# Performance work log

Measured on AMD Instinct MI355X. Metric: run time of the kernel, lower is better.

The kernel has to match this reference:

```python
import jax, jax.numpy as jnp
import numpy as np

B, H, W, C, E, TOP_K = 16, 64, 64, 384, 5, 2


def setup_inputs() -> dict:
    key = jax.random.key(0)
    k1, k2, k3 = jax.random.split(key, 3)
    x = jax.random.normal(k1, (B, H, W, C), dtype=jnp.float32)
    Wg = jax.random.normal(k2, (C, E), dtype=jnp.float32) * 0.02   # router
    We = jax.random.normal(k3, (E, C, C), dtype=jnp.float32) * 0.02  # expert weights
    be = jnp.zeros((E, C), dtype=jnp.float32)                       # expert biases
    return {"x": x, "Wg": Wg, "We": We, "be": be}


def reference(x, Wg, We, be):
    Bx, Hx, Wx, Cx = x.shape
    Ex = Wg.shape[1]
    t = x.reshape(-1, Cx)                      # [N, C] tokens
    N = t.shape[0]

    # --- top-k routing ---
    logits = t @ Wg                            # [N, E]
    top_vals, top_idx = jax.lax.top_k(logits, TOP_K)   # [N, 2]
    gates = jax.nn.softmax(top_vals, axis=-1)          # softmax over selected experts
    combine = jnp.zeros((N, Ex), dtype=t.dtype)
    combine = combine.at[jnp.arange(N)[:, None], top_idx].set(gates)  # [N, E] sparse combine weights

    # --- expert computation (dense over experts, combined with sparse gates) ---
    expert_out = jnp.einsum('nc,ecd->ned', t, We) + be[None]  # [N, E, C]
    y = jnp.einsum('ne,ned->nd', combine, expert_out)         # [N, C]

    # --- LeakyReLU (default slope 0.01); dropout is identity in eval mode ---
    y = jax.nn.leaky_relu(y, negative_slope=0.01)
    return y.reshape(Bx, Hx, Wx, Cx)
```

## Files before the change

kernel.cpp:

```cpp
#include <hip/hip_runtime.h>
#include <stdint.h>

#define TOKENS 65536
#define CDIM 384
#define NEXP 5
#define NPAIR 10
#define CAP 8192
#define NBLK 1024
#define WE_STRIDE (CDIM * CDIM)

typedef __attribute__((ext_vector_type(8))) short short8;
typedef __attribute__((ext_vector_type(4))) float floatx4;

__constant__ int PAIR_A[NPAIR] = {0, 0, 0, 0, 1, 1, 1, 2, 2, 3};
__constant__ int PAIR_B[NPAIR] = {1, 2, 3, 4, 2, 3, 4, 3, 4, 4};

__device__ inline unsigned short f2bf(float f) {
    union { float f; uint32_t u; } v; v.f = f;
    uint32_t r = v.u + 0x7fffu + ((v.u >> 16) & 1u);
    return (unsigned short)(r >> 16);
}

__device__ inline void load_lds16(const void* g, void* l) {
    __builtin_amdgcn_global_load_lds((const __attribute__((address_space(1))) void*)g,
                                     (__attribute__((address_space(3))) void*)l, 16, 0, 0);
}

__global__ __launch_bounds__(256) void router_kernel(const float* __restrict__ x,
                                                     const float* __restrict__ Wg,
                                                     int* __restrict__ blkcnt,
                                                     int* __restrict__ tmeta,
                                                     float2* __restrict__ tgate) {
    __shared__ __align__(16) float  wgs[CDIM * 8];
    __shared__ __align__(16) double part[4 * 64 * NEXP];
    __shared__ __align__(16) double lg[64 * NEXP];
    int t = threadIdx.x, lane = t & 63, w = t >> 6;
    int tok0 = blockIdx.x * 64;

    for (int i = t; i < CDIM * NEXP; i += 256) wgs[(i / NEXP) * 8 + (i % NEXP)] = Wg[i];
    __syncthreads();

    const float4* xb = (const float4*)(x + (size_t)(tok0 + lane) * CDIM + w * 96);
    double p0 = 0, p1 = 0, p2 = 0, p3 = 0, p4 = 0;
    #pragma unroll
    for (int i4 = 0; i4 < 24; ++i4) {
        float4 xv = xb[i4];
        #pragma unroll
        for (int u = 0; u < 4; ++u) {
            int c = w * 96 + i4 * 4 + u;
            float xe = (u == 0) ? xv.x : (u == 1) ? xv.y : (u == 2) ? xv.z : xv.w;
            float4 w03 = *(const float4*)&wgs[c * 8];
            float  w4  = wgs[c * 8 + 4];
            double xd = (double)xe;
            p0 += xd * w03.x; p1 += xd * w03.y; p2 += xd * w03.z;
            p3 += xd * w03.w; p4 += xd * w4;
        }
    }
    double* pr = &part[(w * 64 + lane) * NEXP];
    pr[0] = p0; pr[1] = p1; pr[2] = p2; pr[3] = p3; pr[4] = p4;
    __syncthreads();

    for (int item = t; item < 64 * NEXP; item += 256) {
        lg[item] = part[item] + part[320 + item] + part[640 + item] + part[960 + item];
    }
    __syncthreads();

    if (t < 64) {
        double pa[NEXP];
        #pragma unroll
        for (int e = 0; e < NEXP; ++e) pa[e] = lg[t * NEXP + e];
        int i0 = 0; double m0v = pa[0];
        #pragma unroll
        for (int e = 1; e < NEXP; ++e) if (pa[e] > m0v) { m0v = pa[e]; i0 = e; }
        int i1 = -1; double m1v = -1e300;
        #pragma unroll
        for (int e = 0; e < NEXP; ++e) if (e != i0 && pa[e] > m1v) { m1v = pa[e]; i1 = e; }
        float d  = (float)(m1v - m0v);
        float e1 = expf(d);
        float inv = 1.0f / (1.0f + e1);

        int a  = i0 < i1 ? i0 : i1;
        int b2 = i0 < i1 ? i1 : i0;
        int p  = a * 4 - ((a * (a - 1)) >> 1) + (b2 - a - 1);
        float ga = (a == i0) ? inv : e1 * inv;
        float gb = (a == i0) ? e1 * inv : inv;

        unsigned long long below = (1ull << lane) - 1ull;
        int myrank = 0, myh = 0;
        #pragma unroll
        for (int e = 0; e < NPAIR; ++e) {
            unsigned long long mask = __ballot(p == e);
            if (p == e)    myrank = (int)__popcll(mask & below);
            if (lane == e) myh    = (int)__popcll(mask);
        }
        tmeta[tok0 + lane] = p | (myrank << 8);
        tgate[tok0 + lane] = make_float2(ga, gb);
        if (lane < NPAIR) blkcnt[lane * NBLK + blockIdx.x] = myh;
    }
}

__global__ __launch_bounds__(256) void scan_kernel(const int* __restrict__ blkcnt,
                                                   int* __restrict__ bbase,
                                                   int* __restrict__ cnt) {
    __shared__ int wsum[4];
    int p = blockIdx.x, t = threadIdx.x, lane = t & 63, w = t >> 6;
    int4 v = ((const int4*)(blkcnt + p * NBLK))[t];
    int s0 = v.x, s1 = s0 + v.y, s2 = s1 + v.z, s3 = s2 + v.w;
    int ws = s3;
    #pragma unroll
    for (int d = 1; d < 64; d <<= 1) {
        int o = __shfl_up(ws, d);
        if (lane >= d) ws += o;
    }
    if (lane == 63) wsum[w] = ws;
    __syncthreads();
    int woff = 0;
    for (int k = 0; k < w; ++k) woff += wsum[k];
    int excl = woff + ws - s3;
    int4 b; b.x = excl; b.y = excl + s0; b.z = excl + s1; b.w = excl + s2;
    ((int4*)(bbase + p * NBLK))[t] = b;
    if (t == 255) cnt[p] = excl + s3;
}

__global__ __launch_bounds__(256) void scatter_kernel(const int* __restrict__ tmeta,
                                                      const int* __restrict__ bbase,
                                                      int* __restrict__ bidx) {
    int tok = blockIdx.x * 256 + threadIdx.x;
    int meta = tmeta[tok];
    int p = meta & 255, rank = meta >> 8;
    int pos = bbase[p * NBLK + (tok >> 6)] + rank;
    if (pos < CAP) bidx[p * CAP + pos] = tok;
}

__global__ __launch_bounds__(256) void convert_we(const float* __restrict__ We,
                                                  unsigned short* __restrict__ WeT) {
    __shared__ float tile[64][65];
    int e  = blockIdx.z;
    int c0 = blockIdx.x * 64, d0 = blockIdx.y * 64;
    int t  = threadIdx.x;
    const float* src = We + (size_t)e * WE_STRIDE;
    int dr = t & 15, cr = t >> 4;
    for (int s = 0; s < 64; s += 16) {
        float4 v = *(const float4*)&src[(size_t)(c0 + cr + s) * CDIM + d0 + dr * 4];
        tile[cr + s][dr * 4 + 0] = v.x;
        tile[cr + s][dr * 4 + 1] = v.y;
        tile[cr + s][dr * 4 + 2] = v.z;
        tile[cr + s][dr * 4 + 3] = v.w;
    }
    __syncthreads();
    unsigned short* dst = WeT + (size_t)e * WE_STRIDE;
    int c4 = t & 15, drow = t >> 4;
    for (int s = 0; s < 64; s += 16) {
        int d = drow + s;
        ushort4 o;
        o.x = f2bf(tile[c4 * 4 + 0][d]);
        o.y = f2bf(tile[c4 * 4 + 1][d]);
        o.z = f2bf(tile[c4 * 4 + 2][d]);
        o.w = f2bf(tile[c4 * 4 + 3][d]);
        *(ushort4*)&dst[(size_t)(d0 + d) * CDIM + c0 + c4 * 4] = o;
    }
}

__global__ __launch_bounds__(512, 4) void moe_kernel(const float* __restrict__ x,
                                                     const unsigned short* __restrict__ WeT,
                                                     const int* __restrict__ cnt,
                                                     const int* __restrict__ bidx,
                                                     const float2* __restrict__ tgate,
                                                     const float* __restrict__ be,
                                                     float* __restrict__ out) {
    int bh  = blockIdx.x;
    int bid = (bh & 7) * 240 + (bh >> 3);
    int pq  = bid / 3;
    int nt  = bid - pq * 3;
    int p   = pq >> 6;
    int mt  = pq & 63;

    int nct = cnt[p];
    int m0  = mt * 128;
    if (m0 >= nct) return;
    int valid = nct - m0; if (valid > 128) valid = 128;

    int ea = PAIR_A[p], eb = PAIR_B[p];
    int n0 = nt * 128;
    int t = threadIdx.x, lane = t & 63, wid = t >> 6;
    int wm = wid >> 1, wn = wid & 1;
    int q = lane >> 4, cc = lane & 15;

    __shared__ __align__(16) unsigned short S[3072 * 8];

    floatx4 acc[2][2][4];
    #pragma unroll
    for (int e = 0; e < 2; ++e)
        #pragma unroll
        for (int i = 0; i < 2; ++i)
            #pragma unroll
            for (int j = 0; j < 4; ++j)
                acc[e][i][j] = (floatx4){0.0f, 0.0f, 0.0f, 0.0f};

    int rrow = t >> 2, gp = t & 3;
    int gl = (gp - (rrow >> 1)) & 3;
    const unsigned short* bsrcA = WeT + (size_t)ea * WE_STRIDE + (size_t)(n0 + rrow) * CDIM + gl * 8;
    const unsigned short* bsrcB = WeT + (size_t)eb * WE_STRIDE + (size_t)(n0 + rrow) * CDIM + gl * 8;
    int bdstA = 1024 + wid * 64;
    int bdstB = 1024 + 512 + wid * 64;

    int srow = t >> 2, sp = t & 3;
    int arow = m0 + (srow < valid ? srow : valid - 1);
    int gi = bidx[p * CAP + arow];
    const float* xrow = x + (size_t)gi * CDIM + sp * 8;
    int agr = 4 * srow + ((sp + (srow >> 1)) & 3);

    int perm = (q + (cc >> 1)) & 3;
    int a_gr = 4 * (wm * 32 + cc) + perm;
    int b_gr = 1024 + 4 * (wn * 64 + cc) + perm;

    load_lds16(bsrcA, S + (size_t)bdstA * 8);
    load_lds16(bsrcB, S + (size_t)bdstB * 8);
    float4 xreg[2][2];
    xreg[0][0] = *(const float4*)(xrow);
    xreg[0][1] = *(const float4*)(xrow + 4);

    #pragma unroll
    for (int kc = 0; kc < 12; ++kc) {
        int buf = kc & 1;
        float4 a0 = xreg[buf][0], a1 = xreg[buf][1];
        short8 av;
        av[0] = f2bf(a0.x); av[1] = f2bf(a0.y); av[2] = f2bf(a0.z); av[3] = f2bf(a0.w);
        av[4] = f2bf(a1.x); av[5] = f2bf(a1.y); av[6] = f2bf(a1.z); av[7] = f2bf(a1.w);
        *(short8*)&S[(size_t)(buf * 512 + agr) * 8] = av;

        __syncthreads();

        if (kc < 11) {
            int nb = 1 - buf;
            int k1 = (kc + 1) * 32;
            load_lds16(bsrcA + k1, S + (size_t)(nb * 1024 + bdstA) * 8);
            load_lds16(bsrcB + k1, S + (size_t)(nb * 1024 + bdstB) * 8);
            xreg[nb][0] = *(const float4*)(xrow + k1);
            xreg[nb][1] = *(const float4*)(xrow + k1 + 4);
        }

        int ao = buf * 512, bo = buf * 1024;
        short8 af0 = *(const short8*)&S[(size_t)(ao + a_gr) * 8];
        short8 af1 = *(const short8*)&S[(size_t)(ao + a_gr + 64) * 8];
        #pragma unroll
        for (int e = 0; e < 2; ++e) {
            #pragma unroll
            for (int j = 0; j < 4; ++j) {
                short8 bf = *(const short8*)&S[(size_t)(bo + b_gr + e * 512 + j * 64) * 8];
                acc[e][0][j] = __builtin_amdgcn_mfma_f32_16x16x32_bf16(af0, bf, acc[e][0][j], 0, 0, 0);
                acc[e][1][j] = __builtin_amdgcn_mfma_f32_16x16x32_bf16(af1, bf, acc[e][1][j], 0, 0, 0);
            }
        }
    }

    __syncthreads();
    float2* Gp = (float2*)S;
    int*    Ip = (int*)((char*)S + 1024);
    if (t < 128) {
        int rr = m0 + (t < valid ? t : valid - 1);
        int gid = bidx[p * CAP + rr];
        Ip[t] = gid;
        Gp[t] = tgate[gid];
    }
    float ba_[4], bb_[4];
    #pragma unroll
    for (int j = 0; j < 4; ++j) {
        int oc = n0 + wn * 64 + j * 16 + cc;
        ba_[j] = be[ea * CDIM + oc];
        bb_[j] = be[eb * CDIM + oc];
    }
    __syncthreads();

    #pragma unroll
    for (int i = 0; i < 2; ++i) {
        #pragma unroll
        for (int rr4 = 0; rr4 < 4; ++rr4) {
            int trow = wm * 32 + i * 16 + q * 4 + rr4;
            if (trow < valid) {
                float2 g = Gp[trow];
                int gid  = Ip[trow];
                #pragma unroll
                for (int j = 0; j < 4; ++j) {
                    int oc = n0 + wn * 64 + j * 16 + cc;
                    float v = g.x * (acc[0][i][j][rr4] + ba_[j])
                            + g.y * (acc[1][i][j][rr4] + bb_[j]);
                    v = v > 0.0f ? v : 0.01f * v;
                    out[(size_t)gid * CDIM + oc] = v;
                }
            }
        }
    }
}

extern "C" void kernel_launch(void* const* d_in, const int* in_sizes, int n_in,
                              void* d_out, int out_size, void* d_ws, size_t ws_size,
                              hipStream_t stream) {
    const float* x  = (const float*)d_in[0];
    const float* Wg = (const float*)d_in[1];
    const float* We = (const float*)d_in[2];
    const float* be = (const float*)d_in[3];
    float* out = (float*)d_out;

    char* ws = (char*)d_ws;
    int*            cnt    = (int*)ws;
    int*            bidx   = (int*)(ws + 256);
    int*            blkcnt = (int*)(ws + 327936);
    int*            bbase  = (int*)(ws + 368896);
    int*            tmeta  = (int*)(ws + 409856);
    float2*         tgate  = (float2*)(ws + 672000);
    unsigned short* WeT    = (unsigned short*)(ws + 1196288);

    router_kernel<<<NBLK, 256, 0, stream>>>(x, Wg, blkcnt, tmeta, tgate);
    scan_kernel<<<NPAIR, 256, 0, stream>>>(blkcnt, bbase, cnt);
    scatter_kernel<<<TOKENS / 256, 256, 0, stream>>>(tmeta, bbase, bidx);
    convert_we<<<dim3(6, 6, 5), 256, 0, stream>>>(We, WeT);
    moe_kernel<<<NPAIR * 64 * 3, 512, 0, stream>>>(x, WeT, cnt, bidx, tgate, be, out);
}
```

Before: 250.2 us.

## Triple-buffer expert weight tiles with manual waitcnt; stage router inputs through LDS

The expert GEMM kernel moves from double to triple buffering of the B (weight) tiles in LDS and prefetches two k-steps ahead. The generic __syncthreads is replaced with explicit s_waitcnt vmcnt plus s_barrier, so loads stay in flight across iterations. The router kernel now stages x through a padded LDS tile in coalesced row chunks instead of strided per-lane float4 reads. This costs more LDS per block, which may lower occupancy, and the hand-written waitcnt counts must match the actual number of outstanding loads to stay correct.

```diff
diff --git a/kernel.cpp b/kernel.cpp
--- a/kernel.cpp
+++ b/kernel.cpp
@@ -31,6 +31,7 @@
                                                      int* __restrict__ blkcnt,
                                                      int* __restrict__ tmeta,
                                                      float2* __restrict__ tgate) {
+    __shared__ __align__(16) float  xs[64 * 129];
     __shared__ __align__(16) float  wgs[CDIM * 8];
     __shared__ __align__(16) double part[4 * 64 * NEXP];
     __shared__ __align__(16) double lg[64 * NEXP];
@@ -38,20 +39,27 @@
     int tok0 = blockIdx.x * 64;
 
     for (int i = t; i < CDIM * NEXP; i += 256) wgs[(i / NEXP) * 8 + (i % NEXP)] = Wg[i];
-    __syncthreads();
-
-    const float4* xb = (const float4*)(x + (size_t)(tok0 + lane) * CDIM + w * 96);
+
+    int lrow = t >> 5, loff = (t & 31) * 4;
     double p0 = 0, p1 = 0, p2 = 0, p3 = 0, p4 = 0;
     #pragma unroll
-    for (int i4 = 0; i4 < 24; ++i4) {
-        float4 xv = xb[i4];
-        #pragma unroll
-        for (int u = 0; u < 4; ++u) {
-            int c = w * 96 + i4 * 4 + u;
-            float xe = (u == 0) ? xv.x : (u == 1) ? xv.y : (u == 2) ? xv.z : xv.w;
+    for (int ch = 0; ch < 3; ++ch) {
+        __syncthreads();
+        #pragma unroll
+        for (int r8 = 0; r8 < 8; ++r8) {
+            int row = r8 * 8 + lrow;
+            float4 v = *(const float4*)&x[(size_t)(tok0 + row) * CDIM + ch * 128 + loff];
+            float* d = &xs[row * 129 + loff];
+            d[0] = v.x; d[1] = v.y; d[2] = v.z; d[3] = v.w;
+        }
+        __syncthreads();
+        const float* xr = &xs[lane * 129 + w * 32];
+        #pragma unroll
+        for (int j = 0; j < 32; ++j) {
+            int c = ch * 128 + w * 32 + j;
             float4 w03 = *(const float4*)&wgs[c * 8];
             float  w4  = wgs[c * 8 + 4];
-            double xd = (double)xe;
+            double xd = (double)xr[j];
             p0 += xd * w03.x; p1 += xd * w03.y; p2 += xd * w03.z;
             p3 += xd * w03.w; p4 += xd * w4;
         }
@@ -186,7 +194,7 @@
     int wm = wid >> 1, wn = wid & 1;
     int q = lane >> 4, cc = lane & 15;
 
-    __shared__ __align__(16) unsigned short S[3072 * 8];
+    __shared__ __align__(16) unsigned short S[4096 * 8];
 
     floatx4 acc[2][2][4];
     #pragma unroll
@@ -201,8 +209,8 @@
     int gl = (gp - (rrow >> 1)) & 3;
     const unsigned short* bsrcA = WeT + (size_t)ea * WE_STRIDE + (size_t)(n0 + rrow) * CDIM + gl * 8;
     const unsigned short* bsrcB = WeT + (size_t)eb * WE_STRIDE + (size_t)(n0 + rrow) * CDIM + gl * 8;
-    int bdstA = 1024 + wid * 64;
-    int bdstB = 1024 + 512 + wid * 64;
+    int bdstA = wid * 64;
+    int bdstB = 512 + wid * 64;
 
     int srow = t >> 2, sp = t & 3;
     int arow = m0 + (srow < valid ? srow : valid - 1);
@@ -212,35 +220,46 @@
 
     int perm = (q + (cc >> 1)) & 3;
     int a_gr = 4 * (wm * 32 + cc) + perm;
-    int b_gr = 1024 + 4 * (wn * 64 + cc) + perm;
-
-    load_lds16(bsrcA, S + (size_t)bdstA * 8);
-    load_lds16(bsrcB, S + (size_t)bdstB * 8);
+    int b_gr = 4 * (wn * 64 + cc) + perm;
+
     float4 xreg[2][2];
     xreg[0][0] = *(const float4*)(xrow);
     xreg[0][1] = *(const float4*)(xrow + 4);
+    xreg[1][0] = *(const float4*)(xrow + 32);
+    xreg[1][1] = *(const float4*)(xrow + 36);
+    load_lds16(bsrcA,      S + (size_t)(1024 + bdstA) * 8);
+    load_lds16(bsrcB,      S + (size_t)(1024 + bdstB) * 8);
+    load_lds16(bsrcA + 32, S + (size_t)(2048 + bdstA) * 8);
+    load_lds16(bsrcB + 32, S + (size_t)(2048 + bdstB) * 8);
 
     #pragma unroll
     for (int kc = 0; kc < 12; ++kc) {
         int buf = kc & 1;
+        int bb  = kc - (kc / 3) * 3;
         float4 a0 = xreg[buf][0], a1 = xreg[buf][1];
         short8 av;
         av[0] = f2bf(a0.x); av[1] = f2bf(a0.y); av[2] = f2bf(a0.z); av[3] = f2bf(a0.w);
         av[4] = f2bf(a1.x); av[5] = f2bf(a1.y); av[6] = f2bf(a1.z); av[7] = f2bf(a1.w);
         *(short8*)&S[(size_t)(buf * 512 + agr) * 8] = av;
 
-        __syncthreads();
-
-        if (kc < 11) {
-            int nb = 1 - buf;
-            int k1 = (kc + 1) * 32;
-            load_lds16(bsrcA + k1, S + (size_t)(nb * 1024 + bdstA) * 8);
-            load_lds16(bsrcB + k1, S + (size_t)(nb * 1024 + bdstB) * 8);
-            xreg[nb][0] = *(const float4*)(xrow + k1);
-            xreg[nb][1] = *(const float4*)(xrow + k1 + 4);
-        }
-
-        int ao = buf * 512, bo = buf * 1024;
+        if (kc == 0 || kc == 11) {
+            asm volatile("s_waitcnt vmcnt(0) lgkmcnt(0)" ::: "memory");
+        } else {
+            asm volatile("s_waitcnt vmcnt(4) lgkmcnt(0)" ::: "memory");
+        }
+        __builtin_amdgcn_s_barrier();
+        __builtin_amdgcn_sched_barrier(0);
+
+        if (kc < 10) {
+            int k2 = (kc + 2) * 32;
+            int nb = (kc + 2) % 3;
+            xreg[buf][0] = *(const float4*)(xrow + k2);
+            xreg[buf][1] = *(const float4*)(xrow + k2 + 4);
+            load_lds16(bsrcA + k2, S + (size_t)(1024 + nb * 1024 + bdstA) * 8);
+            load_lds16(bsrcB + k2, S + (size_t)(1024 + nb * 1024 + bdstB) * 8);
+        }
+
+        int ao = buf * 512, bo = 1024 + bb * 1024;
         short8 af0 = *(const short8*)&S[(size_t)(ao + a_gr) * 8];
         short8 af1 = *(const short8*)&S[(size_t)(ao + a_gr + 64) * 8];
         #pragma unroll
```

After: 246.9 us. No clear change (-1.3%).
